# Optimization experiments

Measured on AMD Instinct MI355X. Metric: run time of the kernel, lower is better.

The kernel has to match this reference:

```python
import math
import jax, jax.numpy as jnp
import numpy as np

B, N, C = 512, 196, 384
H, W = 14, 8  # rfft2 half-spectrum of 14x14 grid


def setup_inputs() -> dict:
    key = jax.random.key(0)
    k1, k2 = jax.random.split(key)
    x = jax.random.normal(k1, (B, N, C), dtype=jnp.float32)
    complex_weight = jax.random.normal(k2, (H, W, C, 2), dtype=jnp.float32) * 0.02
    return {"x": x, "complex_weight": complex_weight}


def reference(x, complex_weight):
    b_, n_, c_ = x.shape
    a = int(round(math.sqrt(n_)))  # spatial_size=None -> a = b = sqrt(N)
    xs = x.reshape(b_, a, a, c_).astype(jnp.float32)
    xf = jnp.fft.rfft2(xs, axes=(1, 2), norm="ortho")  # [B, a, a//2+1, C] complex
    w = jax.lax.complex(complex_weight[..., 0], complex_weight[..., 1])
    xf = xf * w
    out = jnp.fft.irfft2(xf, s=(a, a), axes=(1, 2), norm="ortho")
    return out.reshape(b_, n_, c_)
```

## Files before the change

### kernel.cpp

```cpp
#include <hip/hip_runtime.h>

namespace {
constexpr int Bb = 512, Nn = 196, Cc = 384, CT = 16, TPB = 128;
constexpr int RST = 228;
constexpr int USZ = CT * RST;

constexpr float C7t[7] = {1.f, 0.6234898018587335f, -0.2225209339563144f,
                          -0.9009688679024191f, -0.9009688679024191f,
                          -0.2225209339563144f, 0.6234898018587335f};
constexpr float S7t[7] = {0.f, 0.7818314824680298f, 0.9749279121818236f,
                          0.4338837391175581f, -0.4338837391175581f,
                          -0.9749279121818236f, -0.7818314824680298f};
constexpr float C14t[14] = {1.f, 0.9009688679024191f, 0.6234898018587336f, 0.2225209339563144f,
                            -0.2225209339563144f, -0.6234898018587336f, -0.9009688679024191f, -1.f,
                            -0.9009688679024191f, -0.6234898018587336f, -0.2225209339563144f,
                            0.2225209339563144f, 0.6234898018587336f, 0.9009688679024191f};
constexpr float S14t[14] = {0.f, 0.4338837391175581f, 0.7818314824680298f, 0.9749279121818236f,
                            0.9749279121818236f, 0.7818314824680298f, 0.4338837391175581f, 0.f,
                            -0.4338837391175581f, -0.7818314824680298f, -0.9749279121818236f,
                            -0.9749279121818236f, -0.7818314824680298f, -0.4338837391175581f};
}

template<int SG>
__device__ __forceinline__ void dft7(const float* vr, const float* vi, float* Er, float* Ei) {
  const float P1r = vr[1] + vr[6], M1r = vr[1] - vr[6];
  const float P1i = vi[1] + vi[6], M1i = vi[1] - vi[6];
  const float P2r = vr[2] + vr[5], M2r = vr[2] - vr[5];
  const float P2i = vi[2] + vi[5], M2i = vi[2] - vi[5];
  const float P3r = vr[3] + vr[4], M3r = vr[3] - vr[4];
  const float P3i = vi[3] + vi[4], M3i = vi[3] - vi[4];
  Er[0] = vr[0] + P1r + P2r + P3r;
  Ei[0] = vi[0] + P1i + P2i + P3i;
#pragma unroll
  for (int k = 1; k < 7; ++k) {
    const float c1 = C7t[k], c2 = C7t[(2 * k) % 7], c3 = C7t[(3 * k) % 7];
    const float s1 = SG * S7t[k], s2 = SG * S7t[(2 * k) % 7], s3 = SG * S7t[(3 * k) % 7];
    float er = fmaf(P1r, c1, vr[0]);
    er = fmaf(P2r, c2, er);
    er = fmaf(P3r, c3, er);
    er = fmaf(M1i, s1, er);
    er = fmaf(M2i, s2, er);
    er = fmaf(M3i, s3, er);
    float ei = fmaf(P1i, c1, vi[0]);
    ei = fmaf(P2i, c2, ei);
    ei = fmaf(P3i, c3, ei);
    ei = fmaf(M1r, -s1, ei);
    ei = fmaf(M2r, -s2, ei);
    ei = fmaf(M3r, -s3, ei);
    Er[k] = er; Ei[k] = ei;
  }
}

__global__ __launch_bounds__(TPB, 4) void gf_kernel(const float* __restrict__ x,
                                                    const float* __restrict__ wt,
                                                    float* __restrict__ out) {
  __shared__ float U[USZ];
  __shared__ float Ct[14], St[14];

  const int tid = threadIdx.x;
  const int b   = blockIdx.y;
  const int c0  = blockIdx.x * CT;

  if (tid < 14) { Ct[tid] = C14t[tid]; St[tid] = S14t[tid]; }

  const float* xb = x + (size_t)b * (Nn * Cc) + c0;
#pragma unroll
  for (int k = 0; k < 7; ++k) {
    const int i = tid + k * TPB;
    if (i < Nn * 4) {
      const int n = i >> 2, g = (i & 3) << 2;
      const float4 q = *reinterpret_cast<const float4*>(&xb[n * Cc + g]);
      const int u = n / 14;
      float* Un = &U[n + 2 * u];
      Un[(g + 0) * RST] = q.x;
      Un[(g + 1) * RST] = q.y;
      Un[(g + 2) * RST] = q.z;
      Un[(g + 3) * RST] = q.w;
    }
  }
  __syncthreads();

  const int cl = tid & 15;
  const int w  = tid >> 4;

  float cw[7], sw[7];
  {
    int idx = w;
#pragma unroll
    for (int v = 1; v < 7; ++v) {
      cw[v] = Ct[idx]; sw[v] = St[idx];
      idx += w; if (idx >= 14) idx -= 14;
    }
  }
  const float sg = (w & 1) ? -1.f : 1.f;

  float Vr[14], Vi[14];
  const float* Srow = &U[cl * RST];
#pragma unroll
  for (int u = 0; u < 14; ++u) {
    const float4 q0 = *reinterpret_cast<const float4*>(&Srow[u * 16 + 0]);
    const float4 q1 = *reinterpret_cast<const float4*>(&Srow[u * 16 + 4]);
    const float4 q2 = *reinterpret_cast<const float4*>(&Srow[u * 16 + 8]);
    const float4 q3 = *reinterpret_cast<const float4*>(&Srow[u * 16 + 12]);
    const float f0 = fmaf(sg, q1.w, q0.x);
    const float f1 = fmaf(sg, q2.x, q0.y);
    const float f2 = fmaf(sg, q2.y, q0.z);
    const float f3 = fmaf(sg, q2.z, q0.w);
    const float f4 = fmaf(sg, q2.w, q1.x);
    const float f5 = fmaf(sg, q3.x, q1.y);
    const float f6 = fmaf(sg, q3.y, q1.z);
    float vr = f0, vi = 0.f;
    vr = fmaf(f1, cw[1], vr); vi = fmaf(f1, -sw[1], vi);
    vr = fmaf(f2, cw[2], vr); vi = fmaf(f2, -sw[2], vi);
    vr = fmaf(f3, cw[3], vr); vi = fmaf(f3, -sw[3], vi);
    vr = fmaf(f4, cw[4], vr); vi = fmaf(f4, -sw[4], vi);
    vr = fmaf(f5, cw[5], vr); vi = fmaf(f5, -sw[5], vi);
    vr = fmaf(f6, cw[6], vr); vi = fmaf(f6, -sw[6], vi);
    Vr[u] = vr; Vi[u] = vi;
  }

  const float2* wp = reinterpret_cast<const float2*>(wt) + ((size_t)w * Cc + c0 + cl);
  float2 wreg[14];
#pragma unroll
  for (int h = 0; h < 14; ++h) wreg[h] = wp[(size_t)h * (8 * Cc)];

  __syncthreads();

  float evr[7], evi[7], odr[7], odi[7];
#pragma unroll
  for (int t = 0; t < 7; ++t) {
    evr[t] = Vr[2 * t];     evi[t] = Vi[2 * t];
    odr[t] = Vr[2 * t + 1]; odi[t] = Vi[2 * t + 1];
  }
  float Er[7], Ei[7], Qr[7], Qi[7];
  dft7<1>(evr, evi, Er, Ei);
  dft7<1>(odr, odi, Qr, Qi);
  float Xr[14], Xi[14];
  Xr[0] = Er[0] + Qr[0]; Xi[0] = Ei[0] + Qi[0];
  Xr[7] = Er[0] - Qr[0]; Xi[7] = Ei[0] - Qi[0];
#pragma unroll
  for (int h = 1; h < 7; ++h) {
    const float c = C14t[h], s = S14t[h];
    const float Tr = fmaf(Qr[h], c,  Qi[h] * s);
    const float Ti = fmaf(Qi[h], c, -Qr[h] * s);
    Xr[h] = Er[h] + Tr;     Xi[h] = Ei[h] + Ti;
    Xr[h + 7] = Er[h] - Tr; Xi[h + 7] = Ei[h] - Ti;
  }

  const float scale = ((w == 0 || w == 7) ? 1.f : 2.f) / 196.f;
  float Yr[14], Yi[14];
#pragma unroll
  for (int h = 0; h < 14; ++h) {
    const float wr = wreg[h].x, wi = wreg[h].y;
    Yr[h] = (Xr[h] * wr - Xi[h] * wi) * scale;
    Yi[h] = (Xr[h] * wi + Xi[h] * wr) * scale;
  }

#pragma unroll
  for (int t = 0; t < 7; ++t) {
    evr[t] = Yr[2 * t];     evi[t] = Yi[2 * t];
    odr[t] = Yr[2 * t + 1]; odi[t] = Yi[2 * t + 1];
  }
  dft7<-1>(evr, evi, Er, Ei);
  dft7<-1>(odr, odi, Qr, Qi);
  float* Ap = &U[cl * RST + w];
  Ap[0]            = Er[0] + Qr[0];  Ap[8]            = Ei[0] + Qi[0];
  Ap[7 * 16]       = Er[0] - Qr[0];  Ap[7 * 16 + 8]   = Ei[0] - Qi[0];
#pragma unroll
  for (int p = 1; p < 7; ++p) {
    const float c = C14t[p], s = S14t[p];
    const float Tr = fmaf(Qr[p], c, -Qi[p] * s);
    const float Ti = fmaf(Qi[p], c,  Qr[p] * s);
    Ap[p * 16]           = Er[p] + Tr;  Ap[p * 16 + 8]       = Ei[p] + Ti;
    Ap[(p + 7) * 16]     = Er[p] - Tr;  Ap[(p + 7) * 16 + 8] = Ei[p] - Ti;
  }
  __syncthreads();

  float* ob = out + (size_t)b * (Nn * Cc) + c0;
#pragma unroll
  for (int r = 0; r < 2; ++r) {
    const int e = tid + r * TPB;
    if (e < 14 * CT) {
      const int c2 = e & 15, p = e >> 4;
      const float* ap = &U[c2 * RST + p * 16];
      float a[16];
      *reinterpret_cast<float4*>(&a[0])  = *reinterpret_cast<const float4*>(&ap[0]);
      *reinterpret_cast<float4*>(&a[4])  = *reinterpret_cast<const float4*>(&ap[4]);
      *reinterpret_cast<float4*>(&a[8])  = *reinterpret_cast<const float4*>(&ap[8]);
      *reinterpret_cast<float4*>(&a[12]) = *reinterpret_cast<const float4*>(&ap[12]);
      float* op = ob + (p * 14) * Cc + c2;
      op[0]       = ((a[0] + a[7]) + (a[1] + a[2])) + ((a[3] + a[4]) + (a[5] + a[6]));
      op[7 * Cc]  = ((a[0] - a[7]) - (a[1] - a[2])) - ((a[3] - a[4]) + (a[5] - a[6]));
#pragma unroll
      for (int q = 1; q < 7; ++q) {
        float cs = (q & 1) ? (a[0] - a[7]) : (a[0] + a[7]);
        float ss = 0.f;
#pragma unroll
        for (int w2 = 1; w2 < 7; ++w2) {
          cs = fmaf(a[w2], C14t[(w2 * q) % 14], cs);
          ss = fmaf(a[8 + w2], S14t[(w2 * q) % 14], ss);
        }
        op[q * Cc]        = cs - ss;
        op[(14 - q) * Cc] = cs + ss;
      }
    }
  }
}

extern "C" void kernel_launch(void* const* d_in, const int* in_sizes, int n_in,
                              void* d_out, int out_size, void* d_ws, size_t ws_size,
                              hipStream_t stream) {
  const float* x  = (const float*)d_in[0];
  const float* wt = (const float*)d_in[1];
  float* out      = (float*)d_out;
  dim3 grid(Cc / CT, Bb);
  gf_kernel<<<grid, TPB, 0, stream>>>(x, wt, out);
}
```

Baseline: 312.4 us.

## Process four batches per block with double-buffered register-staged prefetch

Each block now handles four batch images with two shared-memory buffers. The next image is loaded from global into registers during the current image's FFT and written to the other buffer, and the complex weights are loaded once per block instead of once per image. The loader also pre-folds the even/odd (n, n+7) butterfly, so the first DFT stage reads only 8 values per row instead of 16. The trade-off is higher register and LDS use: launch bounds drop to 2 blocks per SIMD, and the grid has four times fewer blocks, which may reduce occupancy and latency hiding.

```diff
diff --git a/kernel.cpp b/kernel.cpp
--- a/kernel.cpp
+++ b/kernel.cpp
@@ -1,7 +1,7 @@
 #include <hip/hip_runtime.h>
 
 namespace {
-constexpr int Bb = 512, Nn = 196, Cc = 384, CT = 16, TPB = 128;
+constexpr int Bb = 512, Nn = 196, Cc = 384, CT = 16, TPB = 128, NB = 4;
 constexpr int RST = 228;
 constexpr int USZ = CT * RST;
 
@@ -51,37 +51,66 @@
   }
 }
 
-__global__ __launch_bounds__(TPB, 4) void gf_kernel(const float* __restrict__ x,
+__global__ __launch_bounds__(TPB, 2) void gf_kernel(const float* __restrict__ x,
                                                     const float* __restrict__ wt,
                                                     float* __restrict__ out) {
-  __shared__ float U[USZ];
+  __shared__ float U[2][USZ];
   __shared__ float Ct[14], St[14];
 
   const int tid = threadIdx.x;
-  const int b   = blockIdx.y;
   const int c0  = blockIdx.x * CT;
+  const int b0  = blockIdx.y * NB;
 
   if (tid < 14) { Ct[tid] = C14t[tid]; St[tid] = S14t[tid]; }
-
-  const float* xb = x + (size_t)b * (Nn * Cc) + c0;
-#pragma unroll
-  for (int k = 0; k < 7; ++k) {
-    const int i = tid + k * TPB;
-    if (i < Nn * 4) {
-      const int n = i >> 2, g = (i & 3) << 2;
-      const float4 q = *reinterpret_cast<const float4*>(&xb[n * Cc + g]);
-      const int u = n / 14;
-      float* Un = &U[n + 2 * u];
-      Un[(g + 0) * RST] = q.x;
-      Un[(g + 1) * RST] = q.y;
-      Un[(g + 2) * RST] = q.z;
-      Un[(g + 3) * RST] = q.w;
-    }
-  }
-  __syncthreads();
 
   const int cl = tid & 15;
   const int w  = tid >> 4;
+
+  const float* xb0 = x + (size_t)b0 * (Nn * Cc) + c0;
+  float4 sA[4], sB[4];
+
+  auto stage_load = [&](const float* xb) {
+#pragma unroll
+    for (int k = 0; k < 4; ++k) {
+      const int j = tid + k * TPB;
+      if (j < 392) {
+        const int g_ = (j & 3) << 2;
+        const int pr = j >> 2;
+        const int u  = pr / 7, vp = pr - u * 7;
+        const int n1 = u * 14 + vp;
+        sA[k] = *reinterpret_cast<const float4*>(&xb[n1 * Cc + g_]);
+        sB[k] = *reinterpret_cast<const float4*>(&xb[(n1 + 7) * Cc + g_]);
+      }
+    }
+  };
+  auto stage_write = [&](int buf) {
+#pragma unroll
+    for (int k = 0; k < 4; ++k) {
+      const int j = tid + k * TPB;
+      if (j < 392) {
+        const int g_ = (j & 3) << 2;
+        const int pr = j >> 2;
+        const int u  = pr / 7, vp = pr - u * 7;
+        float* Up = &U[buf][g_ * RST + u * 16 + vp];
+        const float a0 = sA[k].x, e0 = sB[k].x;
+        Up[0]           = a0 + e0;  Up[8]           = a0 - e0;
+        const float a1 = sA[k].y, e1 = sB[k].y;
+        Up[RST]         = a1 + e1;  Up[RST + 8]     = a1 - e1;
+        const float a2 = sA[k].z, e2 = sB[k].z;
+        Up[2 * RST]     = a2 + e2;  Up[2 * RST + 8] = a2 - e2;
+        const float a3 = sA[k].w, e3 = sB[k].w;
+        Up[3 * RST]     = a3 + e3;  Up[3 * RST + 8] = a3 - e3;
+      }
+    }
+  };
+
+  stage_load(xb0);
+  const float2* wp = reinterpret_cast<const float2*>(wt) + ((size_t)w * Cc + c0 + cl);
+  float2 wreg[14];
+#pragma unroll
+  for (int h = 0; h < 14; ++h) wreg[h] = wp[(size_t)h * (8 * Cc)];
+  stage_write(0);
+  __syncthreads();
 
   float cw[7], sw[7];
   {
@@ -92,118 +121,114 @@
       idx += w; if (idx >= 14) idx -= 14;
     }
   }
-  const float sg = (w & 1) ? -1.f : 1.f;
-
-  float Vr[14], Vi[14];
-  const float* Srow = &U[cl * RST];
-#pragma unroll
-  for (int u = 0; u < 14; ++u) {
-    const float4 q0 = *reinterpret_cast<const float4*>(&Srow[u * 16 + 0]);
-    const float4 q1 = *reinterpret_cast<const float4*>(&Srow[u * 16 + 4]);
-    const float4 q2 = *reinterpret_cast<const float4*>(&Srow[u * 16 + 8]);
-    const float4 q3 = *reinterpret_cast<const float4*>(&Srow[u * 16 + 12]);
-    const float f0 = fmaf(sg, q1.w, q0.x);
-    const float f1 = fmaf(sg, q2.x, q0.y);
-    const float f2 = fmaf(sg, q2.y, q0.z);
-    const float f3 = fmaf(sg, q2.z, q0.w);
-    const float f4 = fmaf(sg, q2.w, q1.x);
-    const float f5 = fmaf(sg, q3.x, q1.y);
-    const float f6 = fmaf(sg, q3.y, q1.z);
-    float vr = f0, vi = 0.f;
-    vr = fmaf(f1, cw[1], vr); vi = fmaf(f1, -sw[1], vi);
-    vr = fmaf(f2, cw[2], vr); vi = fmaf(f2, -sw[2], vi);
-    vr = fmaf(f3, cw[3], vr); vi = fmaf(f3, -sw[3], vi);
-    vr = fmaf(f4, cw[4], vr); vi = fmaf(f4, -sw[4], vi);
-    vr = fmaf(f5, cw[5], vr); vi = fmaf(f5, -sw[5], vi);
-    vr = fmaf(f6, cw[6], vr); vi = fmaf(f6, -sw[6], vi);
-    Vr[u] = vr; Vi[u] = vi;
-  }
-
-  const float2* wp = reinterpret_cast<const float2*>(wt) + ((size_t)w * Cc + c0 + cl);
-  float2 wreg[14];
-#pragma unroll
-  for (int h = 0; h < 14; ++h) wreg[h] = wp[(size_t)h * (8 * Cc)];
-
-  __syncthreads();
-
-  float evr[7], evi[7], odr[7], odi[7];
-#pragma unroll
-  for (int t = 0; t < 7; ++t) {
-    evr[t] = Vr[2 * t];     evi[t] = Vi[2 * t];
-    odr[t] = Vr[2 * t + 1]; odi[t] = Vi[2 * t + 1];
-  }
-  float Er[7], Ei[7], Qr[7], Qi[7];
-  dft7<1>(evr, evi, Er, Ei);
-  dft7<1>(odr, odi, Qr, Qi);
-  float Xr[14], Xi[14];
-  Xr[0] = Er[0] + Qr[0]; Xi[0] = Ei[0] + Qi[0];
-  Xr[7] = Er[0] - Qr[0]; Xi[7] = Ei[0] - Qi[0];
-#pragma unroll
-  for (int h = 1; h < 7; ++h) {
-    const float c = C14t[h], s = S14t[h];
-    const float Tr = fmaf(Qr[h], c,  Qi[h] * s);
-    const float Ti = fmaf(Qi[h], c, -Qr[h] * s);
-    Xr[h] = Er[h] + Tr;     Xi[h] = Ei[h] + Ti;
-    Xr[h + 7] = Er[h] - Tr; Xi[h + 7] = Ei[h] - Ti;
-  }
-
+  const int par8 = (w & 1) * 8;
   const float scale = ((w == 0 || w == 7) ? 1.f : 2.f) / 196.f;
-  float Yr[14], Yi[14];
-#pragma unroll
-  for (int h = 0; h < 14; ++h) {
-    const float wr = wreg[h].x, wi = wreg[h].y;
-    Yr[h] = (Xr[h] * wr - Xi[h] * wi) * scale;
-    Yi[h] = (Xr[h] * wi + Xi[h] * wr) * scale;
-  }
-
-#pragma unroll
-  for (int t = 0; t < 7; ++t) {
-    evr[t] = Yr[2 * t];     evi[t] = Yi[2 * t];
-    odr[t] = Yr[2 * t + 1]; odi[t] = Yi[2 * t + 1];
-  }
-  dft7<-1>(evr, evi, Er, Ei);
-  dft7<-1>(odr, odi, Qr, Qi);
-  float* Ap = &U[cl * RST + w];
-  Ap[0]            = Er[0] + Qr[0];  Ap[8]            = Ei[0] + Qi[0];
-  Ap[7 * 16]       = Er[0] - Qr[0];  Ap[7 * 16 + 8]   = Ei[0] - Qi[0];
-#pragma unroll
-  for (int p = 1; p < 7; ++p) {
-    const float c = C14t[p], s = S14t[p];
-    const float Tr = fmaf(Qr[p], c, -Qi[p] * s);
-    const float Ti = fmaf(Qi[p], c,  Qr[p] * s);
-    Ap[p * 16]           = Er[p] + Tr;  Ap[p * 16 + 8]       = Ei[p] + Ti;
-    Ap[(p + 7) * 16]     = Er[p] - Tr;  Ap[(p + 7) * 16 + 8] = Ei[p] - Ti;
-  }
-  __syncthreads();
-
-  float* ob = out + (size_t)b * (Nn * Cc) + c0;
-#pragma unroll
-  for (int r = 0; r < 2; ++r) {
-    const int e = tid + r * TPB;
-    if (e < 14 * CT) {
-      const int c2 = e & 15, p = e >> 4;
-      const float* ap = &U[c2 * RST + p * 16];
-      float a[16];
-      *reinterpret_cast<float4*>(&a[0])  = *reinterpret_cast<const float4*>(&ap[0]);
-      *reinterpret_cast<float4*>(&a[4])  = *reinterpret_cast<const float4*>(&ap[4]);
-      *reinterpret_cast<float4*>(&a[8])  = *reinterpret_cast<const float4*>(&ap[8]);
-      *reinterpret_cast<float4*>(&a[12]) = *reinterpret_cast<const float4*>(&ap[12]);
-      float* op = ob + (p * 14) * Cc + c2;
-      op[0]       = ((a[0] + a[7]) + (a[1] + a[2])) + ((a[3] + a[4]) + (a[5] + a[6]));
-      op[7 * Cc]  = ((a[0] - a[7]) - (a[1] - a[2])) - ((a[3] - a[4]) + (a[5] - a[6]));
-#pragma unroll
-      for (int q = 1; q < 7; ++q) {
-        float cs = (q & 1) ? (a[0] - a[7]) : (a[0] + a[7]);
-        float ss = 0.f;
-#pragma unroll
-        for (int w2 = 1; w2 < 7; ++w2) {
-          cs = fmaf(a[w2], C14t[(w2 * q) % 14], cs);
-          ss = fmaf(a[8 + w2], S14t[(w2 * q) % 14], ss);
+
+  int cur = 0;
+  for (int t = 0; t < NB; ++t) {
+    float Vr[14], Vi[14];
+    const float* Fr = &U[cur][cl * RST + par8];
+#pragma unroll
+    for (int u = 0; u < 14; ++u) {
+      const float4 q0 = *reinterpret_cast<const float4*>(&Fr[u * 16]);
+      const float4 q1 = *reinterpret_cast<const float4*>(&Fr[u * 16 + 4]);
+      float vr = q0.x, vi = 0.f;
+      vr = fmaf(q0.y, cw[1], vr); vi = fmaf(q0.y, -sw[1], vi);
+      vr = fmaf(q0.z, cw[2], vr); vi = fmaf(q0.z, -sw[2], vi);
+      vr = fmaf(q0.w, cw[3], vr); vi = fmaf(q0.w, -sw[3], vi);
+      vr = fmaf(q1.x, cw[4], vr); vi = fmaf(q1.x, -sw[4], vi);
+      vr = fmaf(q1.y, cw[5], vr); vi = fmaf(q1.y, -sw[5], vi);
+      vr = fmaf(q1.z, cw[6], vr); vi = fmaf(q1.z, -sw[6], vi);
+      Vr[u] = vr; Vi[u] = vi;
+    }
+
+    if (t + 1 < NB) stage_load(xb0 + (size_t)(t + 1) * (Nn * Cc));
+
+    __syncthreads();
+
+    float evr[7], evi[7], odr[7], odi[7];
+#pragma unroll
+    for (int i2 = 0; i2 < 7; ++i2) {
+      evr[i2] = Vr[2 * i2];     evi[i2] = Vi[2 * i2];
+      odr[i2] = Vr[2 * i2 + 1]; odi[i2] = Vi[2 * i2 + 1];
+    }
+    float Er[7], Ei[7], Qr[7], Qi[7];
+    dft7<1>(evr, evi, Er, Ei);
+    dft7<1>(odr, odi, Qr, Qi);
+    float Xr[14], Xi[14];
+    Xr[0] = Er[0] + Qr[0]; Xi[0] = Ei[0] + Qi[0];
+    Xr[7] = Er[0] - Qr[0]; Xi[7] = Ei[0] - Qi[0];
+#pragma unroll
+    for (int h = 1; h < 7; ++h) {
+      const float c = C14t[h], s = S14t[h];
+      const float Tr = fmaf(Qr[h], c,  Qi[h] * s);
+      const float Ti = fmaf(Qi[h], c, -Qr[h] * s);
+      Xr[h] = Er[h] + Tr;     Xi[h] = Ei[h] + Ti;
+      Xr[h + 7] = Er[h] - Tr; Xi[h + 7] = Ei[h] - Ti;
+    }
+
+    float Yr[14], Yi[14];
+#pragma unroll
+    for (int h = 0; h < 14; ++h) {
+      const float wr = wreg[h].x, wi = wreg[h].y;
+      Yr[h] = (Xr[h] * wr - Xi[h] * wi) * scale;
+      Yi[h] = (Xr[h] * wi + Xi[h] * wr) * scale;
+    }
+
+#pragma unroll
+    for (int i2 = 0; i2 < 7; ++i2) {
+      evr[i2] = Yr[2 * i2];     evi[i2] = Yi[2 * i2];
+      odr[i2] = Yr[2 * i2 + 1]; odi[i2] = Yi[2 * i2 + 1];
+    }
+    dft7<-1>(evr, evi, Er, Ei);
+    dft7<-1>(odr, odi, Qr, Qi);
+    float* Ap = &U[cur][cl * RST + w];
+    Ap[0]          = Er[0] + Qr[0];  Ap[8]          = Ei[0] + Qi[0];
+    Ap[7 * 16]     = Er[0] - Qr[0];  Ap[7 * 16 + 8] = Ei[0] - Qi[0];
+#pragma unroll
+    for (int p = 1; p < 7; ++p) {
+      const float c = C14t[p], s = S14t[p];
+      const float Tr = fmaf(Qr[p], c, -Qi[p] * s);
+      const float Ti = fmaf(Qi[p], c,  Qr[p] * s);
+      Ap[p * 16]           = Er[p] + Tr;  Ap[p * 16 + 8]       = Ei[p] + Ti;
+      Ap[(p + 7) * 16]     = Er[p] - Tr;  Ap[(p + 7) * 16 + 8] = Ei[p] - Ti;
+    }
+
+    if (t + 1 < NB) stage_write(cur ^ 1);
+
+    __syncthreads();
+
+    float* ob = out + (size_t)(b0 + t) * (Nn * Cc) + c0;
+#pragma unroll
+    for (int r = 0; r < 2; ++r) {
+      const int e = tid + r * TPB;
+      if (e < 14 * CT) {
+        const int c2 = e & 15, p = e >> 4;
+        const float* ap = &U[cur][c2 * RST + p * 16];
+        float a[16];
+        *reinterpret_cast<float4*>(&a[0])  = *reinterpret_cast<const float4*>(&ap[0]);
+        *reinterpret_cast<float4*>(&a[4])  = *reinterpret_cast<const float4*>(&ap[4]);
+        *reinterpret_cast<float4*>(&a[8])  = *reinterpret_cast<const float4*>(&ap[8]);
+        *reinterpret_cast<float4*>(&a[12]) = *reinterpret_cast<const float4*>(&ap[12]);
+        float* op = ob + (p * 14) * Cc + c2;
+        op[0]       = ((a[0] + a[7]) + (a[1] + a[2])) + ((a[3] + a[4]) + (a[5] + a[6]));
+        op[7 * Cc]  = ((a[0] - a[7]) - (a[1] - a[2])) - ((a[3] - a[4]) + (a[5] - a[6]));
+#pragma unroll
+        for (int q = 1; q < 7; ++q) {
+          float cs = (q & 1) ? (a[0] - a[7]) : (a[0] + a[7]);
+          float ss = 0.f;
+#pragma unroll
+          for (int w2 = 1; w2 < 7; ++w2) {
+            cs = fmaf(a[w2], C14t[(w2 * q) % 14], cs);
+            ss = fmaf(a[8 + w2], S14t[(w2 * q) % 14], ss);
+          }
+          op[q * Cc]        = cs - ss;
+          op[(14 - q) * Cc] = cs + ss;
         }
-        op[q * Cc]        = cs - ss;
-        op[(14 - q) * Cc] = cs + ss;
       }
     }
+
+    cur ^= 1;
   }
 }
 
@@ -213,6 +238,6 @@
   const float* x  = (const float*)d_in[0];
   const float* wt = (const float*)d_in[1];
   float* out      = (float*)d_out;
-  dim3 grid(Cc / CT, Bb);
+  dim3 grid(Cc / CT, Bb / NB);
   gf_kernel<<<grid, TPB, 0, stream>>>(x, wt, out);
 }
```

Result: no change. 306.5 us (-1.9%).
